# Kernel tuning notes

Hardware: AMD Instinct MI355X
Metric: run time of the kernel (lower is better)

## Reference

```python
import jax, jax.numpy as jnp
import numpy as np

N = 4096          # flattened batch*seq tokens
V = 32000         # tgt_vocab_size
LS = 0.1          # label_smoothing
CONF = 1.0 - LS   # confidence mass on gold token
SM = LS / (V - 1) # smoothing mass per non-gold token
IGNORE = -1
PAD = 0


def setup_inputs() -> dict:
    key = jax.random.key(0)
    k1, k2 = jax.random.split(key)
    output = jax.random.normal(k1, (N, V), dtype=jnp.float32)
    target = jax.random.randint(k2, (N,), 0, V, dtype=jnp.int32)
    return {"output": output, "target": target}


def reference(output, target):
    n, v = output.shape
    valid = (target != IGNORE)                       # all True for generated data; kept for fidelity
    tgt = jnp.where(valid, target, PAD)
    validf = valid.astype(output.dtype)
    rows = jnp.arange(n)

    # label-smoothed KL term
    logp = jax.nn.log_softmax(output, axis=-1)       # (N, V)
    model_prob = jnp.full((n, v), SM, dtype=logp.dtype).at[rows, tgt].set(CONF)
    kl_row = jnp.sum(model_prob * (jnp.log(model_prob) - logp), axis=-1)
    loss = jnp.sum(kl_row * validf)

    # unlikelihood term: previous-context tokens as negative candidates
    full = jnp.broadcast_to(tgt[None, :], (n, n))    # (N, N)
    ctx_l = jnp.tril(full, -1)                       # strictly-lower = preceding targets
    ctx_u = ctx_l + PAD
    ctx_u = ctx_u * jnp.triu(ctx_u)                  # faithful to torch construction
    ctx = ctx_l + ctx_u
    ctx = jnp.where(ctx == tgt[:, None], PAD, ctx)   # don't penalize the gold token
    neg = jnp.zeros((n, v), dtype=logp.dtype).at[rows[:, None], ctx].set(1.0)
    neg = neg.at[:, PAD].set(0.0)                    # (N, V) negative-target mask

    one_minus = jnp.clip(1.0 - jnp.exp(logp), 1e-5, None)
    custom_row = jnp.sum(-jnp.log(one_minus) * neg, axis=-1)
    custom = jnp.sum(custom_row * validf)

    norm = jnp.sum((valid & (tgt != PAD)).astype(logp.dtype))
    return loss / norm + 0.1 * custom / norm
```

## Files before the change

kernel.cpp:

```cpp
#include <hip/hip_runtime.h>
#include <math.h>

#define NROWS 4096
#define VCOLS 32000
#define NV4   (VCOLS / 4)

typedef float f32x4 __attribute__((ext_vector_type(4)));

constexpr float CONF_F   = 0.9f;
constexpr float SM_F     = 0.1f / 31999.0f;
constexpr float KL_CONST = -1.36242896f;
constexpr float COEF_T   = CONF_F - SM_F;

__global__ void k_init(int* __restrict__ ft32) {
    int v = blockIdx.x * blockDim.x + threadIdx.x;
    if (v < VCOLS) ft32[v] = NROWS;
}

__global__ void k_scatter(const int* __restrict__ target,
                          int* __restrict__ ft32) {
    int j = blockIdx.x * blockDim.x + threadIdx.x;
    if (j < NROWS) {
        int t  = target[j];
        int tc = (t != -1) ? t : 0;
        if (tc != 0) atomicMin(&ft32[tc], j);
    }
}

__global__ void k_pack(const int* __restrict__ ft32,
                       unsigned short* __restrict__ ft16) {
    int v = blockIdx.x * blockDim.x + threadIdx.x;
    if (v < VCOLS) ft16[v] = (unsigned short)ft32[v];
}

__global__ __launch_bounds__(1024)
void k_main(const float* __restrict__ X,
            const int*   __restrict__ target,
            const unsigned short* __restrict__ ft16,
            float* __restrict__ kl_rows,
            float* __restrict__ custom_rows) {
    const int i   = blockIdx.x;
    const int tid = threadIdx.x;

    __shared__ float cand[NROWS];
    __shared__ float rm[1024], rz[1024], rs[1024];
    __shared__ float s_logZ, s_xt;

    const int t = target[i];
    if (t == -1) {
        if (tid == 0) { kl_rows[i] = 0.0f; custom_rows[i] = 0.0f; }
        return;
    }
    const int    mytgt = t;
    const float* row   = X + (size_t)i * VCOLS;

    if (tid == 0) s_xt = row[mytgt];
    for (int j = tid; j < i; j += 1024) cand[j] = -INFINITY;
    __syncthreads();

    const f32x4* row4 = (const f32x4*)row;
    const int2*  ft2  = (const int2*)ft16;

    float m = -INFINITY, Z = 0.0f, sx = 0.0f;

#define SLOT(ee_) do {                                                        \
        const int e_ = (ee_);                                                 \
        f32x4 x_ = row4[e_];                                                  \
        int2  f_ = ft2[e_];                                                   \
        float m4_ = fmaxf(fmaxf(x_.x, x_.y), fmaxf(x_.z, x_.w));              \
        float mn_ = fmaxf(m, m4_);                                            \
        Z = Z * __expf(m - mn_)                                               \
          + __expf(x_.x - mn_) + __expf(x_.y - mn_)                           \
          + __expf(x_.z - mn_) + __expf(x_.w - mn_);                          \
        m = mn_;                                                              \
        sx += (x_.x + x_.y) + (x_.z + x_.w);                                  \
        int b_  = e_ * 4;                                                     \
        int a0_ = f_.x & 0xFFFF, a1_ = (int)(((unsigned)f_.x) >> 16);         \
        int a2_ = f_.y & 0xFFFF, a3_ = (int)(((unsigned)f_.y) >> 16);         \
        if (a0_ < i && b_     != mytgt) cand[a0_] = x_.x;                     \
        if (a1_ < i && b_ + 1 != mytgt) cand[a1_] = x_.y;                     \
        if (a2_ < i && b_ + 2 != mytgt) cand[a2_] = x_.z;                     \
        if (a3_ < i && b_ + 3 != mytgt) cand[a3_] = x_.w;                     \
    } while (0)

    int e = tid;
    while (e + 1024 < NV4) { SLOT(e); SLOT(e + 1024); e += 2048; }
    if (e < NV4) SLOT(e);
#undef SLOT

    rm[tid] = m; rz[tid] = Z; rs[tid] = sx;
    __syncthreads();
    for (int s = 512; s > 0; s >>= 1) {
        if (tid < s) {
            float m2 = rm[tid + s], z2 = rz[tid + s];
            float mm = fmaxf(rm[tid], m2);
            rz[tid]  = rz[tid] * __expf(rm[tid] - mm) + z2 * __expf(m2 - mm);
            rm[tid]  = mm;
            rs[tid] += rs[tid + s];
        }
        __syncthreads();
    }
    if (tid == 0) {
        float logZ    = rm[0] + __logf(rz[0]);
        s_logZ        = logZ;
        float logp_t  = s_xt - logZ;
        float sumlogp = rs[0] - (float)VCOLS * logZ;
        kl_rows[i] = KL_CONST - COEF_T * logp_t - SM_F * sumlogp;
    }
    __syncthreads();
    const float logZ = s_logZ;

    float acc = 0.0f;
    for (int j = tid; j < i; j += 1024) {
        float xv = cand[j];
        float p  = __expf(xv - logZ);
        float om = fmaxf(1.0f - p, 1e-5f);
        acc -= __logf(om);
    }
    rs[tid] = acc;
    __syncthreads();
    for (int s = 512; s > 0; s >>= 1) {
        if (tid < s) rs[tid] += rs[tid + s];
        __syncthreads();
    }
    if (tid == 0) custom_rows[i] = rs[0];
}

__global__ __launch_bounds__(1024)
void k_final(const float* __restrict__ kl_rows,
             const float* __restrict__ custom_rows,
             const int*   __restrict__ target,
             float* __restrict__ out) {
    __shared__ float sl[1024], sc[1024], sn[1024];
    int tid = threadIdx.x;
    float L = 0.0f, C = 0.0f, Nn = 0.0f;
    for (int j = tid; j < NROWS; j += 1024) {
        L += kl_rows[j];
        C += custom_rows[j];
        int t = target[j];
        if (t != -1 && t != 0) Nn += 1.0f;
    }
    sl[tid] = L; sc[tid] = C; sn[tid] = Nn;
    __syncthreads();
    for (int s = 512; s > 0; s >>= 1) {
        if (tid < s) { sl[tid] += sl[tid+s]; sc[tid] += sc[tid+s]; sn[tid] += sn[tid+s]; }
        __syncthreads();
    }
    if (tid == 0) {
        float norm = sn[0];
        out[0] = sl[0] / norm + 0.1f * sc[0] / norm;
    }
}

extern "C" void kernel_launch(void* const* d_in, const int* in_sizes, int n_in,
                              void* d_out, int out_size, void* d_ws, size_t ws_size,
                              hipStream_t stream) {
    const float* X      = (const float*)d_in[0];
    const int*   target = (const int*)d_in[1];
    float*       out    = (float*)d_out;

    char* ws = (char*)d_ws;
    int*            ft32        = (int*)           (ws);
    unsigned short* ft16        = (unsigned short*)(ws + 128000);
    float*          kl_rows     = (float*)         (ws + 192000);
    float*          custom_rows = (float*)         (ws + 192000 + 16384);

    k_init   <<<(VCOLS + 255) / 256, 256, 0, stream>>>(ft32);
    k_scatter<<<(NROWS + 255) / 256, 256, 0, stream>>>(target, ft32);
    k_pack   <<<(VCOLS + 255) / 256, 256, 0, stream>>>(ft32, ft16);
    k_main   <<<NROWS,              1024, 0, stream>>>(X, target, ft16,
                                                       kl_rows, custom_rows);
    k_final  <<<1,                  1024, 0, stream>>>(kl_rows, custom_rows, target, out);
}
```

Baseline: 123.9 us.

## Shrink main block to 256 threads and software-pipeline row loads

Cuts the per-row block from 1024 to 256 threads, so each thread now processes about 31 float4 elements instead of 8. Loads for the next pair of chunks are issued before the current pair is processed, and the online softmax rescale runs once per 8 values instead of once per 4. The goal is more memory-level parallelism per thread, fewer rescale exponentials, and cheaper block reductions and barriers. In exchange it raises register pressure and leaves fewer threads per block to hide latency.

```diff
diff --git a/kernel.cpp b/kernel.cpp
--- a/kernel.cpp
+++ b/kernel.cpp
@@ -33,7 +33,7 @@
     if (v < VCOLS) ft16[v] = (unsigned short)ft32[v];
 }
 
-__global__ __launch_bounds__(1024)
+__global__ __launch_bounds__(256)
 void k_main(const float* __restrict__ X,
             const int*   __restrict__ target,
             const unsigned short* __restrict__ ft16,
@@ -43,7 +43,7 @@
     const int tid = threadIdx.x;
 
     __shared__ float cand[NROWS];
-    __shared__ float rm[1024], rz[1024], rs[1024];
+    __shared__ float rm[256], rz[256], rs[256];
     __shared__ float s_logZ, s_xt;
 
     const int t = target[i];
@@ -55,7 +55,7 @@
     const float* row   = X + (size_t)i * VCOLS;
 
     if (tid == 0) s_xt = row[mytgt];
-    for (int j = tid; j < i; j += 1024) cand[j] = -INFINITY;
+    for (int j = tid; j < i; j += 256) cand[j] = -INFINITY;
     __syncthreads();
 
     const f32x4* row4 = (const f32x4*)row;
@@ -63,34 +63,64 @@
 
     float m = -INFINITY, Z = 0.0f, sx = 0.0f;
 
-#define SLOT(ee_) do {                                                        \
-        const int e_ = (ee_);                                                 \
-        f32x4 x_ = row4[e_];                                                  \
-        int2  f_ = ft2[e_];                                                   \
-        float m4_ = fmaxf(fmaxf(x_.x, x_.y), fmaxf(x_.z, x_.w));              \
-        float mn_ = fmaxf(m, m4_);                                            \
-        Z = Z * __expf(m - mn_)                                               \
-          + __expf(x_.x - mn_) + __expf(x_.y - mn_)                           \
-          + __expf(x_.z - mn_) + __expf(x_.w - mn_);                          \
-        m = mn_;                                                              \
-        sx += (x_.x + x_.y) + (x_.z + x_.w);                                  \
-        int b_  = e_ * 4;                                                     \
-        int a0_ = f_.x & 0xFFFF, a1_ = (int)(((unsigned)f_.x) >> 16);         \
-        int a2_ = f_.y & 0xFFFF, a3_ = (int)(((unsigned)f_.y) >> 16);         \
-        if (a0_ < i && b_     != mytgt) cand[a0_] = x_.x;                     \
-        if (a1_ < i && b_ + 1 != mytgt) cand[a1_] = x_.y;                     \
-        if (a2_ < i && b_ + 2 != mytgt) cand[a2_] = x_.z;                     \
-        if (a3_ < i && b_ + 3 != mytgt) cand[a3_] = x_.w;                     \
+#define MAX4(xx_) fmaxf(fmaxf((xx_).x, (xx_).y), fmaxf((xx_).z, (xx_).w))
+#define SCAT(xx_, ff_, ee_) do {                                              \
+        int base_ = (ee_) * 4;                                                \
+        int a0_ = (ff_).x & 0xFFFF, a1_ = (int)(((unsigned)(ff_).x) >> 16);   \
+        int a2_ = (ff_).y & 0xFFFF, a3_ = (int)(((unsigned)(ff_).y) >> 16);   \
+        unsigned d_ = (unsigned)(mytgt - base_);                              \
+        if (a0_ < i && d_ != 0u) cand[a0_] = (xx_).x;                         \
+        if (a1_ < i && d_ != 1u) cand[a1_] = (xx_).y;                         \
+        if (a2_ < i && d_ != 2u) cand[a2_] = (xx_).z;                         \
+        if (a3_ < i && d_ != 3u) cand[a3_] = (xx_).w;                         \
     } while (0)
+#define CHUNK(xa_, fa_, xb_, fb_, ea_) do {                                   \
+        float cm_ = fmaxf(MAX4(xa_), MAX4(xb_));                              \
+        float mn_ = fmaxf(m, cm_);                                            \
+        Z *= __expf(m - mn_);                         \
+        m  = mn_;                                                             \
+        Z += __expf((xa_).x - m) + __expf((xa_).y - m)                        \
+           + __expf((xa_).z - m) + __expf((xa_).w - m)                        \
+           + __expf((xb_).x - m) + __expf((xb_).y - m)                        \
+           + __expf((xb_).z - m) + __expf((xb_).w - m);                       \
+        sx += ((xa_).x + (xa_).y) + ((xa_).z + (xa_).w)                       \
+            + ((xb_).x + (xb_).y) + ((xb_).z + (xb_).w);                      \
+        SCAT(xa_, fa_, (ea_));                                                \
+        SCAT(xb_, fb_, (ea_) + 256);                                          \
+    } while (0)
 
     int e = tid;
-    while (e + 1024 < NV4) { SLOT(e); SLOT(e + 1024); e += 2048; }
-    if (e < NV4) SLOT(e);
-#undef SLOT
+    f32x4 xa = row4[e];        int2 fa = ft2[e];
+    f32x4 xb = row4[e + 256];  int2 fb = ft2[e + 256];
+    int en = e + 512;
+
+    while (en + 256 < NV4) {
+        f32x4 xc = row4[en];        int2 fc = ft2[en];
+        f32x4 xd = row4[en + 256];  int2 fd = ft2[en + 256];
+        CHUNK(xa, fa, xb, fb, e);
+        xa = xc; fa = fc; xb = xd; fb = fd;
+        e = en; en += 512;
+    }
+    CHUNK(xa, fa, xb, fb, e);
+
+    for (; en < NV4; en += 256) {
+        f32x4 x_ = row4[en];  int2 f_ = ft2[en];
+        float m4 = MAX4(x_);
+        float mn = fmaxf(m, m4);
+        Z *= __expf(m - mn);
+        m  = mn;
+        Z += __expf(x_.x - m) + __expf(x_.y - m)
+           + __expf(x_.z - m) + __expf(x_.w - m);
+        sx += (x_.x + x_.y) + (x_.z + x_.w);
+        SCAT(x_, f_, en);
+    }
+#undef CHUNK
+#undef SCAT
+#undef MAX4
 
     rm[tid] = m; rz[tid] = Z; rs[tid] = sx;
     __syncthreads();
-    for (int s = 512; s > 0; s >>= 1) {
+    for (int s = 128; s > 0; s >>= 1) {
         if (tid < s) {
             float m2 = rm[tid + s], z2 = rz[tid + s];
             float mm = fmaxf(rm[tid], m2);
@@ -111,7 +141,7 @@
     const float logZ = s_logZ;
 
     float acc = 0.0f;
-    for (int j = tid; j < i; j += 1024) {
+    for (int j = tid; j < i; j += 256) {
         float xv = cand[j];
         float p  = __expf(xv - logZ);
         float om = fmaxf(1.0f - p, 1e-5f);
@@ -119,7 +149,7 @@
     }
     rs[tid] = acc;
     __syncthreads();
-    for (int s = 512; s > 0; s >>= 1) {
+    for (int s = 128; s > 0; s >>= 1) {
         if (tid < s) rs[tid] += rs[tid + s];
         __syncthreads();
     }
@@ -168,7 +198,7 @@
     k_init   <<<(VCOLS + 255) / 256, 256, 0, stream>>>(ft32);
     k_scatter<<<(NROWS + 255) / 256, 256, 0, stream>>>(target, ft32);
     k_pack   <<<(VCOLS + 255) / 256, 256, 0, stream>>>(ft32, ft16);
-    k_main   <<<NROWS,              1024, 0, stream>>>(X, target, ft16,
+    k_main   <<<NROWS,               256, 0, stream>>>(X, target, ft16,
                                                        kl_rows, custom_rows);
     k_final  <<<1,                  1024, 0, stream>>>(kl_rows, custom_rows, target, out);
 }
```

New measurement: 110.0 us. 11.2% less time.
